# Kernel tuning notes

Measured on AMD Instinct MI355X. Metric: run time of the kernel, lower is better.

Reference implementation:

```python
import jax, jax.numpy as jnp
import numpy as np

M = 16          # max number of instance ids (0 = background)
DELTA_AGG = 0.5
DELTA_DIS = 3.0


def setup_inputs() -> dict:
    key = jax.random.key(0)
    k1, k2 = jax.random.split(key)
    preds = jax.random.normal(k1, (8, 6, 640, 640), dtype=jnp.float32)
    targets = jax.random.randint(k2, (8, 2, 640, 640), 0, M).astype(jnp.int32)
    return {"preds": preds, "targets": targets}


def _seg_sum(vals, ids):
    # vals: [P] or [P, C], ids: [P] -> segment sums with M segments
    return jax.ops.segment_sum(vals, ids, num_segments=M)


def reference(preds, targets):
    N = preds.shape[0]
    sim = preds[:, 2:, :, :].reshape(N, 4, -1).transpose(0, 2, 1)  # N x P x 4
    text = targets[:, 0].reshape(N, -1)                            # N x P
    kern = targets[:, 1].reshape(N, -1)                            # N x P
    P = sim.shape[1]

    seg = jax.vmap(_seg_sum)
    ones = jnp.ones((N, P), sim.dtype)
    cnt_k = seg(ones, kern)                         # N x M kernel pixel counts
    cnt_t = seg(ones, text)                         # N x M text pixel counts
    G = seg(sim, kern) / jnp.maximum(cnt_k, 1.0)[..., None]  # N x M x 4, G_Ki means

    inst = jnp.arange(M)
    valid = (cnt_k > 0) & (cnt_t > 0) & (inst[None, :] >= 1)  # N x M (skip id 0)
    nv = jnp.sum(valid, axis=1)                                # N, number of valid instances

    # ---- aggregation loss: per text pixel, distance to its instance's kernel mean
    G_t = jnp.take_along_axis(G, text[..., None], axis=1)      # N x P x 4
    d = jnp.linalg.norm(sim - G_t, axis=-1) - DELTA_AGG        # N x P
    l = jnp.log(jnp.square(jnp.maximum(d, 0.0)) + 1.0)         # N x P
    l_mean = seg(l, text) / jnp.maximum(cnt_t, 1.0)            # N x M per-instance mean
    agg = jnp.sum(jnp.where(valid, l_mean, 0.0), axis=1) / jnp.maximum(nv, 1)

    # ---- discrimination loss: pairwise distances between valid kernel means
    pair = valid[:, :, None] & valid[:, None, :] & ~jnp.eye(M, dtype=bool)[None]
    sq = jnp.sum(jnp.square(G[:, :, None, :] - G[:, None, :, :]), axis=-1)  # N x M x M
    dist = jnp.sqrt(jnp.where(pair, sq, 1.0))
    lp = jnp.where(pair, jnp.log(jnp.square(jnp.maximum(DELTA_DIS - dist, 0.0)) + 1.0), 0.0)
    dis = jnp.where(nv > 1, 0.5 * jnp.sum(lp, axis=(1, 2)) / jnp.maximum(nv * (nv - 1), 1), 0.0)

    return agg.astype(jnp.float32), dis.astype(jnp.float32)
```

## Files before the change

### kernel.cpp

```cpp
#include <hip/hip_runtime.h>
#include <math.h>

#define NB 8
#define MSEG 16
#define PPIX (640*640)
#define PV4 (PPIX/4)
#define GRIDX 128
#define STRIDE (GRIDX*256)
#define FULLCOV (3*STRIDE)
#define DELTA_AGG 0.5f
#define DELTA_DIS 3.0f

typedef float v2f __attribute__((ext_vector_type(2)));

#define OFF_A1 0
#define OFF_A2 (NB*80)
#define WS_ZERO_FLOATS (NB*112)

__global__ __launch_bounds__(256, 3) void pass1_kernel(
    const float* __restrict__ preds, const int* __restrict__ targets,
    float* __restrict__ ws) {
  const int n = blockIdx.y, blk = blockIdx.x;
  const int tid = threadIdx.x, lane = tid & 63, w = tid >> 6;

  const float4* __restrict__ pc0 = (const float4*)(preds + ((size_t)n*6 + 2)*PPIX);
  const float4* __restrict__ pc1 = (const float4*)(preds + ((size_t)n*6 + 3)*PPIX);
  const float4* __restrict__ pc2 = (const float4*)(preds + ((size_t)n*6 + 4)*PPIX);
  const float4* __restrict__ pc3 = (const float4*)(preds + ((size_t)n*6 + 5)*PPIX);
  const int4*  __restrict__ kernv = (const int4*)(targets + ((size_t)n*2 + 1)*PPIX);

  v2f acc01[MSEG], acc23[MSEG];
  float cntk[MSEG];
#pragma unroll
  for (int m = 0; m < MSEG; ++m) {
    acc01[m] = (v2f){0.f, 0.f}; acc23[m] = (v2f){0.f, 0.f}; cntk[m] = 0.f;
  }

#define PIX1(K, A0, A1, A2, A3) do {                                \
    int k_ = (K);                                                   \
    v2f p01 = {(A0), (A1)}, p23 = {(A2), (A3)};                     \
    _Pragma("unroll")                                               \
    for (int m = 1; m < MSEG; ++m) {                                \
      float fk = (k_ == m) ? 1.0f : 0.0f;                           \
      v2f fk2 = {fk, fk};                                           \
      acc01[m] = __builtin_elementwise_fma(fk2, p01, acc01[m]);     \
      acc23[m] = __builtin_elementwise_fma(fk2, p23, acc23[m]);     \
      cntk[m] += fk;                                                \
    } } while (0)

#define GRP1(KK, VA, VB, VC, VD) do {                \
    PIX1((KK).x, (VA).x, (VB).x, (VC).x, (VD).x);    \
    PIX1((KK).y, (VA).y, (VB).y, (VC).y, (VD).y);    \
    PIX1((KK).z, (VA).z, (VB).z, (VC).z, (VD).z);    \
    PIX1((KK).w, (VA).w, (VB).w, (VC).w, (VD).w);    \
  } while (0)

  const int base = blk*256 + tid;
  int4 kc = kernv[base];
  float4 va = pc0[base], vb = pc1[base], vc = pc2[base], vd = pc3[base];
  {
    const int p = base + STRIDE;
    int4 kn = kernv[p];
    float4 an = pc0[p], bn = pc1[p], cn = pc2[p], dn = pc3[p];
    GRP1(kc, va, vb, vc, vd);
    kc = kn; va = an; vb = bn; vc = cn; vd = dn;
  }
  {
    const int p = base + 2*STRIDE;
    int4 kn = kernv[p];
    float4 an = pc0[p], bn = pc1[p], cn = pc2[p], dn = pc3[p];
    GRP1(kc, va, vb, vc, vd);
    kc = kn; va = an; vb = bn; vc = cn; vd = dn;
  }
  {
    int4 kr; float4 ar, br, cr, dr;
    const int pr = FULLCOV + blk*32 + (tid & 31);
    if (tid < 32) { kr = kernv[pr]; ar = pc0[pr]; br = pc1[pr]; cr = pc2[pr]; dr = pc3[pr]; }
    GRP1(kc, va, vb, vc, vd);
    if (tid < 32) GRP1(kr, ar, br, cr, dr);
  }
#undef GRP1
#undef PIX1

  float acc[80];
#pragma unroll
  for (int m = 0; m < MSEG; ++m) {
    acc[m]      = acc01[m].x;
    acc[16 + m] = acc01[m].y;
    acc[32 + m] = acc23[m].x;
    acc[48 + m] = acc23[m].y;
    acc[64 + m] = cntk[m];
  }

#pragma unroll
  for (int s = 0; s < 6; ++s) {
    const int dist = 32 >> s;
    const bool hi = (lane & dist) != 0;
#pragma unroll
    for (int v = 0; v < (32 >> s); ++v) {
      float keep = hi ? acc[v + (32 >> s)] : acc[v];
      float send = hi ? acc[v] : acc[v + (32 >> s)];
      acc[v] = keep + __shfl_xor(send, dist);
    }
  }
  float cn16[16];
#pragma unroll
  for (int m = 0; m < MSEG; ++m) cn16[m] = acc[64 + m];
#pragma unroll
  for (int s = 0; s < 4; ++s) {
    const int dist = 32 >> s;
    const int half = 8 >> s;
    const bool hi = (lane & dist) != 0;
#pragma unroll
    for (int v = 0; v < half; ++v) {
      float keep = hi ? cn16[v + half] : cn16[v];
      float send = hi ? cn16[v] : cn16[v + half];
      cn16[v] = keep + __shfl_xor(send, dist);
    }
  }
  float ckt = cn16[0];
  ckt += __shfl_xor(ckt, 2);
  ckt += __shfl_xor(ckt, 1);

  __shared__ float s_v[4][64];
  __shared__ float s_c[4][16];
  s_v[w][lane] = acc[0];
  if ((lane & 3) == 0) s_c[w][lane >> 2] = ckt;
  __syncthreads();

  if (tid < 64) {
    atomicAdd(&ws[OFF_A1 + n*80 + tid],
              s_v[0][tid] + s_v[1][tid] + s_v[2][tid] + s_v[3][tid]);
  } else if (tid < 80) {
    int i = tid - 64;
    atomicAdd(&ws[OFF_A1 + n*80 + tid],
              s_c[0][i] + s_c[1][i] + s_c[2][i] + s_c[3][i]);
  }
}

__global__ __launch_bounds__(256, 4) void pass2_kernel(
    const float* __restrict__ preds, const int* __restrict__ targets,
    float* __restrict__ ws) {
  const int n = blockIdx.y, blk = blockIdx.x;
  const int tid = threadIdx.x, lane = tid & 63, w = tid >> 6;

  const float4* __restrict__ pc0 = (const float4*)(preds + ((size_t)n*6 + 2)*PPIX);
  const float4* __restrict__ pc1 = (const float4*)(preds + ((size_t)n*6 + 3)*PPIX);
  const float4* __restrict__ pc2 = (const float4*)(preds + ((size_t)n*6 + 4)*PPIX);
  const float4* __restrict__ pc3 = (const float4*)(preds + ((size_t)n*6 + 5)*PPIX);
  const int4*  __restrict__ textv = (const int4*)(targets + (size_t)n*2*PPIX);

  const int base = blk*256 + tid;
  int4 tc = textv[base];
  float4 va = pc0[base], vb = pc1[base], vc = pc2[base], vd = pc3[base];

  __shared__ float s_raw[80];
  __shared__ float4 s_G[MSEG];
  if (tid < 80) s_raw[tid] = ws[OFF_A1 + n*80 + tid];
  __syncthreads();
  if (tid < 64) {
    int ch = tid >> 4, m = tid & 15;
    ((float*)&s_G[m])[ch] = s_raw[tid] / fmaxf(s_raw[64 + m], 1.0f);
  }
  __syncthreads();

  v2f lc[MSEG];
#pragma unroll
  for (int m = 0; m < MSEG; ++m) lc[m] = (v2f){0.f, 0.f};

#define PIX2(T, A0, A1, A2, A3) do {                            \
    int t_ = (T);                                               \
    float4 gv = s_G[t_];                                        \
    float dx = (A0) - gv.x, dy = (A1) - gv.y;                   \
    float dz = (A2) - gv.z, dw = (A3) - gv.w;                   \
    float sq = fmaf(dx, dx, fmaf(dy, dy, fmaf(dz, dz, dw*dw))); \
    float dd = fmaxf(__fsqrt_rn(sq) - DELTA_AGG, 0.f);          \
    float l = __logf(fmaf(dd, dd, 1.f));                        \
    v2f l1 = {l, 1.0f};                                         \
    _Pragma("unroll")                                           \
    for (int m = 1; m < MSEG; ++m) {                            \
      float fk = (t_ == m) ? 1.0f : 0.0f;                       \
      v2f fk2 = {fk, fk};                                       \
      lc[m] = __builtin_elementwise_fma(fk2, l1, lc[m]);        \
    } } while (0)

#define GRP2(TT, VA, VB, VC, VD) do {                \
    PIX2((TT).x, (VA).x, (VB).x, (VC).x, (VD).x);    \
    PIX2((TT).y, (VA).y, (VB).y, (VC).y, (VD).y);    \
    PIX2((TT).z, (VA).z, (VB).z, (VC).z, (VD).z);    \
    PIX2((TT).w, (VA).w, (VB).w, (VC).w, (VD).w);    \
  } while (0)

  {
    const int p = base + STRIDE;
    int4 tn = textv[p];
    float4 an = pc0[p], bn = pc1[p], cn = pc2[p], dn = pc3[p];
    GRP2(tc, va, vb, vc, vd);
    tc = tn; va = an; vb = bn; vc = cn; vd = dn;
  }
  {
    const int p = base + 2*STRIDE;
    int4 tn = textv[p];
    float4 an = pc0[p], bn = pc1[p], cn = pc2[p], dn = pc3[p];
    GRP2(tc, va, vb, vc, vd);
    tc = tn; va = an; vb = bn; vc = cn; vd = dn;
  }
  {
    int4 tr; float4 ar, br, cr, dr;
    const int pr = FULLCOV + blk*32 + (tid & 31);
    if (tid < 32) { tr = textv[pr]; ar = pc0[pr]; br = pc1[pr]; cr = pc2[pr]; dr = pc3[pr]; }
    GRP2(tc, va, vb, vc, vd);
    if (tid < 32) GRP2(tr, ar, br, cr, dr);
  }
#undef GRP2
#undef PIX2

  float ls[MSEG], ct[MSEG];
#pragma unroll
  for (int m = 0; m < MSEG; ++m) { ls[m] = lc[m].x; ct[m] = lc[m].y; }

  float t0, t1;
#pragma unroll
  for (int s = 0; s < 4; ++s) {
    const int dist = 32 >> s; const int half = 8 >> s;
    const bool hi = (lane & dist) != 0;
#pragma unroll
    for (int v = 0; v < half; ++v) {
      float keep = hi ? ls[v + half] : ls[v];
      float send = hi ? ls[v] : ls[v + half];
      ls[v] = keep + __shfl_xor(send, dist);
    }
  }
  t0 = ls[0]; t0 += __shfl_xor(t0, 2); t0 += __shfl_xor(t0, 1);
#pragma unroll
  for (int s = 0; s < 4; ++s) {
    const int dist = 32 >> s; const int half = 8 >> s;
    const bool hi = (lane & dist) != 0;
#pragma unroll
    for (int v = 0; v < half; ++v) {
      float keep = hi ? ct[v + half] : ct[v];
      float send = hi ? ct[v] : ct[v + half];
      ct[v] = keep + __shfl_xor(send, dist);
    }
  }
  t1 = ct[0]; t1 += __shfl_xor(t1, 2); t1 += __shfl_xor(t1, 1);

  __shared__ float s_l[4][16];
  __shared__ float s_t[4][16];
  if ((lane & 3) == 0) { s_l[w][lane >> 2] = t0; s_t[w][lane >> 2] = t1; }
  __syncthreads();

  if (tid < 16)
    atomicAdd(&ws[OFF_A2 + n*32 + tid],
              s_l[0][tid] + s_l[1][tid] + s_l[2][tid] + s_l[3][tid]);
  else if (tid < 32) {
    int i = tid - 16;
    atomicAdd(&ws[OFF_A2 + n*32 + tid],
              s_t[0][i] + s_t[1][i] + s_t[2][i] + s_t[3][i]);
  }
}

__global__ __launch_bounds__(256) void finalize2_kernel(
    const float* __restrict__ ws, float* __restrict__ out) {
  const int n = blockIdx.x;
  const int tid = threadIdx.x;

  __shared__ float raw1[80];
  __shared__ float s2[32];
  __shared__ float sG[MSEG][4];
  __shared__ int   sval[MSEG];
  __shared__ int   snv;
  __shared__ float red[256];
  __shared__ float agg_sum;

  if (tid < 80) raw1[tid] = ws[OFF_A1 + n*80 + tid];
  else if (tid >= 96 && tid < 128) s2[tid - 96] = ws[OFF_A2 + n*32 + (tid - 96)];
  __syncthreads();
  if (tid < 64) {
    int ch = tid >> 4, m = tid & 15;
    sG[m][ch] = raw1[ch*16 + m] / fmaxf(raw1[64 + m], 1.0f);
  }
  if (tid < MSEG)
    sval[tid] = (tid >= 1) && (raw1[64 + tid] > 0.f) && (s2[16 + tid] > 0.f);
  __syncthreads();
  if (tid == 0) { int nv = 0; for (int m = 0; m < MSEG; m++) nv += sval[m]; snv = nv; }

  float av = 0.f;
  if (tid < MSEG && sval[tid]) av = s2[tid] / fmaxf(s2[16 + tid], 1.0f);
  red[tid] = av;
  __syncthreads();
  for (int s = 128; s > 0; s >>= 1) {
    if (tid < s) red[tid] += red[tid + s];
    __syncthreads();
  }
  if (tid == 0) agg_sum = red[0];
  __syncthreads();

  float lp = 0.f;
  {
    int i = tid >> 4, j = tid & 15;
    if (i != j && sval[i] && sval[j]) {
      float dx = sG[i][0] - sG[j][0];
      float dy = sG[i][1] - sG[j][1];
      float dz = sG[i][2] - sG[j][2];
      float dw = sG[i][3] - sG[j][3];
      float dist = sqrtf(dx*dx + dy*dy + dz*dz + dw*dw);
      float t = fmaxf(DELTA_DIS - dist, 0.f);
      lp = logf(t*t + 1.f);
    }
  }
  red[tid] = lp;
  __syncthreads();
  for (int s = 128; s > 0; s >>= 1) {
    if (tid < s) red[tid] += red[tid + s];
    __syncthreads();
  }
  if (tid == 0) {
    int nv = snv;
    out[n] = agg_sum / (float)(nv > 1 ? nv : 1);
    out[NB + n] = (nv > 1) ? 0.5f * red[0] / (float)(nv * (nv - 1)) : 0.f;
  }
}

extern "C" void kernel_launch(void* const* d_in, const int* in_sizes, int n_in,
                              void* d_out, int out_size, void* d_ws, size_t ws_size,
                              hipStream_t stream) {
  const float* preds   = (const float*)d_in[0];
  const int*   targets = (const int*)d_in[1];
  float* out = (float*)d_out;
  float* ws  = (float*)d_ws;

  hipMemsetAsync(d_ws, 0, WS_ZERO_FLOATS * sizeof(float), stream);

  dim3 grid(GRIDX, NB);
  pass1_kernel<<<grid, 256, 0, stream>>>(preds, targets, ws);
  pass2_kernel<<<grid, 256, 0, stream>>>(preds, targets, ws);
  finalize2_kernel<<<NB, 256, 0, stream>>>(ws, out);
}
```

Baseline: 55.56 us.

## Fuse both passes into one persistent kernel with per-image grid barrier

Merges pass1 (per-instance kernel means) and pass2 (aggregation loss) into one kernel. Each block spins on a per-image atomic counter until all blocks of that image have added their partial sums, then starts the second pass. The grid shrinks to 80x8 blocks, each covering five strides with no remainder, so all 640 blocks can be resident at once and the barrier cannot deadlock. This removes a kernel launch and the gap between launches, at the cost of the spin wait and the assumption that every block is co-resident.

```diff
diff --git a/kernel.cpp b/kernel.cpp
--- a/kernel.cpp
+++ b/kernel.cpp
@@ -5,9 +5,8 @@
 #define MSEG 16
 #define PPIX (640*640)
 #define PV4 (PPIX/4)
-#define GRIDX 128
+#define GRIDX 80
 #define STRIDE (GRIDX*256)
-#define FULLCOV (3*STRIDE)
 #define DELTA_AGG 0.5f
 #define DELTA_DIS 3.0f
 
@@ -15,11 +14,12 @@
 
 #define OFF_A1 0
 #define OFF_A2 (NB*80)
-#define WS_ZERO_FLOATS (NB*112)
-
-__global__ __launch_bounds__(256, 3) void pass1_kernel(
+#define OFF_CTR (NB*112)
+#define WS_ZERO_BYTES ((NB*112 + NB) * 4)
+
+__global__ __launch_bounds__(256, 3) void fused_kernel(
     const float* __restrict__ preds, const int* __restrict__ targets,
-    float* __restrict__ ws) {
+    float* __restrict__ ws, int* __restrict__ ctr) {
   const int n = blockIdx.y, blk = blockIdx.x;
   const int tid = threadIdx.x, lane = tid & 63, w = tid >> 6;
 
@@ -27,7 +27,10 @@
   const float4* __restrict__ pc1 = (const float4*)(preds + ((size_t)n*6 + 3)*PPIX);
   const float4* __restrict__ pc2 = (const float4*)(preds + ((size_t)n*6 + 4)*PPIX);
   const float4* __restrict__ pc3 = (const float4*)(preds + ((size_t)n*6 + 5)*PPIX);
+  const int4*  __restrict__ textv = (const int4*)(targets + (size_t)n*2*PPIX);
   const int4*  __restrict__ kernv = (const int4*)(targets + ((size_t)n*2 + 1)*PPIX);
+
+  const int base = blk*256 + tid;
 
   v2f acc01[MSEG], acc23[MSEG];
   float cntk[MSEG];
@@ -55,29 +58,19 @@
     PIX1((KK).w, (VA).w, (VB).w, (VC).w, (VD).w);    \
   } while (0)
 
-  const int base = blk*256 + tid;
-  int4 kc = kernv[base];
-  float4 va = pc0[base], vb = pc1[base], vc = pc2[base], vd = pc3[base];
   {
-    const int p = base + STRIDE;
-    int4 kn = kernv[p];
-    float4 an = pc0[p], bn = pc1[p], cn = pc2[p], dn = pc3[p];
-    GRP1(kc, va, vb, vc, vd);
-    kc = kn; va = an; vb = bn; vc = cn; vd = dn;
-  }
-  {
-    const int p = base + 2*STRIDE;
-    int4 kn = kernv[p];
-    float4 an = pc0[p], bn = pc1[p], cn = pc2[p], dn = pc3[p];
-    GRP1(kc, va, vb, vc, vd);
-    kc = kn; va = an; vb = bn; vc = cn; vd = dn;
-  }
-  {
-    int4 kr; float4 ar, br, cr, dr;
-    const int pr = FULLCOV + blk*32 + (tid & 31);
-    if (tid < 32) { kr = kernv[pr]; ar = pc0[pr]; br = pc1[pr]; cr = pc2[pr]; dr = pc3[pr]; }
-    GRP1(kc, va, vb, vc, vd);
-    if (tid < 32) GRP1(kr, ar, br, cr, dr);
+    int4 kc = kernv[base];
+    float4 va = pc0[base], vb = pc1[base], vc = pc2[base], vd = pc3[base];
+#pragma unroll
+    for (int it = 0; it < 5; ++it) {
+      int4 kn; float4 an, bn, cn, dn;
+      if (it < 4) {
+        const int p = base + (it + 1)*STRIDE;
+        kn = kernv[p]; an = pc0[p]; bn = pc1[p]; cn = pc2[p]; dn = pc3[p];
+      }
+      GRP1(kc, va, vb, vc, vd);
+      if (it < 4) { kc = kn; va = an; vb = bn; vc = cn; vd = dn; }
+    }
   }
 #undef GRP1
 #undef PIX1
@@ -136,23 +129,20 @@
     atomicAdd(&ws[OFF_A1 + n*80 + tid],
               s_c[0][i] + s_c[1][i] + s_c[2][i] + s_c[3][i]);
   }
-}
-
-__global__ __launch_bounds__(256, 4) void pass2_kernel(
-    const float* __restrict__ preds, const int* __restrict__ targets,
-    float* __restrict__ ws) {
-  const int n = blockIdx.y, blk = blockIdx.x;
-  const int tid = threadIdx.x, lane = tid & 63, w = tid >> 6;
-
-  const float4* __restrict__ pc0 = (const float4*)(preds + ((size_t)n*6 + 2)*PPIX);
-  const float4* __restrict__ pc1 = (const float4*)(preds + ((size_t)n*6 + 3)*PPIX);
-  const float4* __restrict__ pc2 = (const float4*)(preds + ((size_t)n*6 + 4)*PPIX);
-  const float4* __restrict__ pc3 = (const float4*)(preds + ((size_t)n*6 + 5)*PPIX);
-  const int4*  __restrict__ textv = (const int4*)(targets + (size_t)n*2*PPIX);
-
-  const int base = blk*256 + tid;
+
   int4 tc = textv[base];
   float4 va = pc0[base], vb = pc1[base], vc = pc2[base], vd = pc3[base];
+
+  __threadfence();
+  __shared__ int s_go;
+  if (tid == 0) {
+    atomicAdd(&ctr[n], 1);
+    while (__hip_atomic_load(&ctr[n], __ATOMIC_ACQUIRE, __HIP_MEMORY_SCOPE_AGENT) < GRIDX)
+      __builtin_amdgcn_s_sleep(8);
+    s_go = 1;
+  }
+  __syncthreads();
+  __threadfence();
 
   __shared__ float s_raw[80];
   __shared__ float4 s_G[MSEG];
@@ -191,26 +181,15 @@
     PIX2((TT).w, (VA).w, (VB).w, (VC).w, (VD).w);    \
   } while (0)
 
-  {
-    const int p = base + STRIDE;
-    int4 tn = textv[p];
-    float4 an = pc0[p], bn = pc1[p], cn = pc2[p], dn = pc3[p];
+#pragma unroll
+  for (int it = 0; it < 5; ++it) {
+    int4 tn; float4 an, bn, cn, dn;
+    if (it < 4) {
+      const int p = base + (it + 1)*STRIDE;
+      tn = textv[p]; an = pc0[p]; bn = pc1[p]; cn = pc2[p]; dn = pc3[p];
+    }
     GRP2(tc, va, vb, vc, vd);
-    tc = tn; va = an; vb = bn; vc = cn; vd = dn;
-  }
-  {
-    const int p = base + 2*STRIDE;
-    int4 tn = textv[p];
-    float4 an = pc0[p], bn = pc1[p], cn = pc2[p], dn = pc3[p];
-    GRP2(tc, va, vb, vc, vd);
-    tc = tn; va = an; vb = bn; vc = cn; vd = dn;
-  }
-  {
-    int4 tr; float4 ar, br, cr, dr;
-    const int pr = FULLCOV + blk*32 + (tid & 31);
-    if (tid < 32) { tr = textv[pr]; ar = pc0[pr]; br = pc1[pr]; cr = pc2[pr]; dr = pc3[pr]; }
-    GRP2(tc, va, vb, vc, vd);
-    if (tid < 32) GRP2(tr, ar, br, cr, dr);
+    if (it < 4) { tc = tn; va = an; vb = bn; vc = cn; vd = dn; }
   }
 #undef GRP2
 #undef PIX2
@@ -329,11 +308,11 @@
   const int*   targets = (const int*)d_in[1];
   float* out = (float*)d_out;
   float* ws  = (float*)d_ws;
-
-  hipMemsetAsync(d_ws, 0, WS_ZERO_FLOATS * sizeof(float), stream);
+  int*   ctr = ((int*)d_ws) + OFF_CTR;
+
+  hipMemsetAsync(d_ws, 0, WS_ZERO_BYTES, stream);
 
   dim3 grid(GRIDX, NB);
-  pass1_kernel<<<grid, 256, 0, stream>>>(preds, targets, ws);
-  pass2_kernel<<<grid, 256, 0, stream>>>(preds, targets, ws);
+  fused_kernel<<<grid, 256, 0, stream>>>(preds, targets, ws, ctr);
   finalize2_kernel<<<NB, 256, 0, stream>>>(ws, out);
 }
```

After: 214.8 us. 3.87x slower.
